# Optimization experiments

Hardware: AMD Instinct MI355X
Metric: run time of the kernel (lower is better)

## Reference

```python
import jax, jax.numpy as jnp
import numpy as np

K = 100  # low-rank dimension


def setup_inputs() -> dict:
    key = jax.random.key(0)
    k1, k2 = jax.random.split(key)
    N, D = 100000, 512
    X = jax.random.normal(k1, (N, D), dtype=jnp.float32)
    # xavier-normal init for Linear(d, 4k): std = sqrt(2/(fan_in+fan_out))
    std = np.sqrt(2.0 / (D + 4 * K)).astype(np.float32)
    W = jax.random.normal(k2, (4 * K, D), dtype=jnp.float32) * std
    b = jnp.zeros((4 * K,), dtype=jnp.float32)
    return {"X": X, "W": W, "b": b}


def reference(X, W, b):
    # tmp = ReLU(X @ W^T + b): [N, 4k]
    tmp = jax.nn.relu(X @ W.T + b)
    U = tmp[:, :K]            # [N, k]
    V = tmp[:, K:2 * K]       # [N, k]
    Z = tmp[:, 2 * K:3 * K]   # [N, k]
    T = tmp[:, 3 * K:]        # [N, k]
    N_rows = X.shape[0]
    # joint_normalize2: sum(U @ (V^T @ ones)) / N + 1e-6 == <colsum(U), colsum(V)> / N + 1e-6
    norm_factor = jnp.dot(jnp.sum(U, axis=0), jnp.sum(V, axis=0)) / N_rows + 1e-6
    Dscale = 1.0 / norm_factor
    # low-rank attention: U @ (V^T @ Z) via small [k, k] intermediate
    VtZ = jnp.einsum('nk,nj->kj', V, Z)   # [k, k]
    res = (U @ VtZ) * Dscale              # [N, k]
    out = jnp.concatenate([res, T], axis=1)  # [N, 2k]
    # dropout p=0.0 (eval-equivalent): identity
    return out
```

## Files before the change

### kernel.cpp

```cpp
#include <hip/hip_runtime.h>
#include <cstdint>

typedef __bf16 bf16;
typedef __attribute__((ext_vector_type(8))) __bf16 bf16x8;
typedef __attribute__((ext_vector_type(4))) __bf16 bf16x4;
typedef __attribute__((ext_vector_type(4))) float f32x4;

#define NROWS 100000
#define DIM   512
#define NC    400
#define NBLK2 521

#define WS_WP    0u
#define WS_SUMU  458752u
#define WS_SUMV  459152u
#define WS_DSC   459552u
#define WS_VTZT  459776u
#define WS_U     524288u
#define WS_PART  66124288u
#define WS_SUMP  71041536u
#define WS_NEED  72291936u

__device__ __forceinline__ void gload_lds16(const void* g, void* l) {
  __builtin_amdgcn_global_load_lds(
      (const __attribute__((address_space(1))) uint32_t*)g,
      (__attribute__((address_space(3))) uint32_t*)l,
      16, 0, 0);
}

__global__ void k1_prep(const float* __restrict__ W, bf16* __restrict__ wp,
                        float* __restrict__ sums) {
  const int idx = blockIdx.x * 256 + threadIdx.x;
  if (idx < 200) sums[idx] = 0.f;
  if (idx >= 16 * 4 * 448 * 8) return;
  const int e = idx & 7;
  int r = idx >> 3;
  const int col = r % 448; r /= 448;
  const int g = r & 3;
  const int t = r >> 2;
  const int k = t * 32 + 4 * g + ((e < 4) ? e : (12 + e));
  wp[idx] = (bf16)((col < NC) ? W[col * DIM + k] : 0.f);
}

__global__ __launch_bounds__(1024) void k2_main(
    const float* __restrict__ X, const bf16* __restrict__ Wp,
    const float* __restrict__ bias, float* __restrict__ out,
    bf16* __restrict__ U, float* __restrict__ part, float* __restrict__ sumP) {
  __shared__ __align__(16) char pool[131072];
  char* Abase0 = pool;
  char* Bbase0 = pool + 73728;

  const int tid  = threadIdx.x;
  const int lane = tid & 63;
  const int wave = tid >> 6;
  const int wm = wave >> 2;
  const int wn = wave & 3;
  const int m  = lane & 15;
  const int g  = lane >> 4;
  const int rb = blockIdx.x * 192;

  f32x4 acc[3][7];
#pragma unroll
  for (int i = 0; i < 3; ++i)
#pragma unroll
    for (int j = 0; j < 7; ++j) acc[i][j] = (f32x4){0.f, 0.f, 0.f, 0.f};

  const int nba = (wave < 8) ? 2 : 1;
  const int ca0 = (wave < 8) ? wave * 2 : 16 + (wave - 8);
  const size_t swb = (size_t)(((lane & 7) ^ (lane >> 3)) * 16);
  int gr0 = rb + ca0 * 8 + (lane >> 3);       if (gr0 > NROWS - 1) gr0 = NROWS - 1;
  int gr1 = rb + (ca0 + 1) * 8 + (lane >> 3); if (gr1 > NROWS - 1) gr1 = NROWS - 1;
  const char* asrc0 = (const char*)X + (size_t)gr0 * 2048 + swb;
  const char* asrc1 = (const char*)X + (size_t)gr1 * 2048 + swb;
  const int nbc = (wave < 12) ? 2 : 1;
  const int bc0 = (wave < 12) ? wave * 2 : 24 + (wave - 12);
  const char* wpc = (const char*)Wp;

#define STAGE_A(T, BUF)                                                        \
  do {                                                                         \
    char* ad = Abase0 + (BUF) * 24576 + ca0 * 1024 + lane * 16;                \
    gload_lds16(asrc0 + (size_t)(T) * 128, ad);                                \
    if (nba == 2) gload_lds16(asrc1 + (size_t)(T) * 128, ad + 1024);           \
  } while (0)
#define STAGE_B(T, BUF)                                                        \
  do {                                                                         \
    const char* bsrc = wpc + (size_t)(T) * 28672;                              \
    for (int q = 0; q < nbc; ++q)                                              \
      gload_lds16(bsrc + (bc0 + q) * 1024 + lane * 16,                         \
                  Bbase0 + (BUF) * 28672 + (bc0 + q) * 1024);                  \
  } while (0)

  STAGE_A(0, 0);
  STAGE_B(0, 0);
  STAGE_A(1, 1);

#pragma unroll
  for (int t = 0; t < 16; ++t) {
    const int ab  = t % 3;
    const int bb_ = t & 1;
    if (t < 15) STAGE_B(t + 1, bb_ ^ 1);
    if (t < 14) STAGE_A(t + 2, (t + 2) % 3);
    if (t < 14) {
      if (wave < 8)       asm volatile("s_waitcnt vmcnt(6)\n\ts_barrier" ::: "memory");
      else if (wave < 12) asm volatile("s_waitcnt vmcnt(4)\n\ts_barrier" ::: "memory");
      else                asm volatile("s_waitcnt vmcnt(3)\n\ts_barrier" ::: "memory");
    } else if (t == 14) {
      if (wave < 8)       asm volatile("s_waitcnt vmcnt(4)\n\ts_barrier" ::: "memory");
      else if (wave < 12) asm volatile("s_waitcnt vmcnt(3)\n\ts_barrier" ::: "memory");
      else                asm volatile("s_waitcnt vmcnt(2)\n\ts_barrier" ::: "memory");
    } else {
      asm volatile("s_waitcnt vmcnt(0)\n\ts_barrier" ::: "memory");
    }

    const int sw = (m & 7) * 16;
    const char* abuf = Abase0 + ab * 24576;
    bf16x8 af[3];
#pragma unroll
    for (int mf = 0; mf < 3; ++mf) {
      const char* rowp = abuf + (wm * 48 + mf * 16 + m) * 128;
      f32x4 alo = *(const f32x4*)(rowp + ((16 * g) ^ sw));
      f32x4 ahi = *(const f32x4*)(rowp + ((64 + 16 * g) ^ sw));
      af[mf] = (bf16x8){(bf16)alo.x, (bf16)alo.y, (bf16)alo.z, (bf16)alo.w,
                        (bf16)ahi.x, (bf16)ahi.y, (bf16)ahi.z, (bf16)ahi.w};
    }

    const bf16* Bc = (const bf16*)(Bbase0 + bb_ * 28672);
#pragma unroll
    for (int nf = 0; nf < 7; ++nf) {
      const int n = wn * 112 + nf * 16 + m;
      bf16x8 bfr = *(const bf16x8*)(Bc + (g * 448 + n) * 8);
#pragma unroll
      for (int mf = 0; mf < 3; ++mf)
        acc[mf][nf] = __builtin_amdgcn_mfma_f32_16x16x32_bf16(af[mf], bfr, acc[mf][nf], 0, 0, 0);
    }
    asm volatile("s_barrier" ::: "memory");
  }
#undef STAGE_A
#undef STAGE_B

  bf16* ldsVZ = (bf16*)pool;
  float* sp   = (float*)(pool + 89600);
  float csum[7];
#pragma unroll
  for (int nf = 0; nf < 7; ++nf) csum[nf] = 0.f;

#pragma unroll
  for (int mf = 0; mf < 3; ++mf) {
#pragma unroll
    for (int nf = 0; nf < 7; ++nf) {
      const int c = wn * 112 + nf * 16 + m;
      const float bv = (c < NC) ? bias[c] : 0.f;
      const int rl0 = wm * 48 + mf * 16 + 4 * g;
      bf16 vz[4];
#pragma unroll
      for (int r = 0; r < 4; ++r) {
        const int row = rb + rl0 + r;
        float v = fmaxf(acc[mf][nf][r] + bv, 0.f);
        const float v2 = (row < NROWS) ? v : 0.f;
        if (row < NROWS) {
          if (c < 100) U[(size_t)row * 128 + c] = (bf16)v;
          if (c >= 300 && c < NC) out[(size_t)row * 200 + 100 + (c - 300)] = v;
        }
        vz[r] = (bf16)v2;
        if (c < 200) csum[nf] += v2;
      }
      if (c >= 100 && c < 300) {
        const int vr = (c < 200) ? (c - 100) : (112 + (c - 200));
        *(bf16x4*)&ldsVZ[(size_t)vr * 200 + rl0] = (bf16x4){vz[0], vz[1], vz[2], vz[3]};
      }
    }
  }
  for (int i = tid; i < 4800; i += 1024) {
    const int rr = (i < 2400) ? (100 + i / 200) : (212 + (i - 2400) / 200);
    ldsVZ[(size_t)rr * 200 + (i % 200)] = (bf16)0.f;
  }
#pragma unroll
  for (int nf = 0; nf < 7; ++nf) {
    float s = csum[nf];
    s += __shfl_xor(s, 16, 64);
    s += __shfl_xor(s, 32, 64);
    if (lane < 16) sp[wave * 112 + nf * 16 + lane] = s;
  }
  __syncthreads();

  if (wave < 7) {
    f32x4 acc2[7];
#pragma unroll
    for (int j = 0; j < 7; ++j) acc2[j] = (f32x4){0.f, 0.f, 0.f, 0.f};
    const bf16* vA = ldsVZ + (size_t)(wave * 16 + m) * 200;
#pragma unroll
    for (int kc = 0; kc < 6; ++kc) {
      bf16x4 a0 = *(const bf16x4*)(vA + kc * 32 + 4 * g);
      bf16x4 a1 = *(const bf16x4*)(vA + kc * 32 + 16 + 4 * g);
      bf16x8 af_ = {a0[0], a0[1], a0[2], a0[3], a1[0], a1[1], a1[2], a1[3]};
#pragma unroll
      for (int fj = 0; fj < 7; ++fj) {
        const bf16* vB = ldsVZ + (size_t)(112 + fj * 16 + m) * 200 + kc * 32;
        bf16x4 b0 = *(const bf16x4*)(vB + 4 * g);
        bf16x4 b1 = *(const bf16x4*)(vB + 16 + 4 * g);
        bf16x8 bf_ = {b0[0], b0[1], b0[2], b0[3], b1[0], b1[1], b1[2], b1[3]};
        acc2[fj] = __builtin_amdgcn_mfma_f32_16x16x32_bf16(af_, bf_, acc2[fj], 0, 0, 0);
      }
    }
    float* pb = part + (size_t)(blockIdx.x % 98) * 12544;
#pragma unroll
    for (int fj = 0; fj < 7; ++fj)
#pragma unroll
      for (int r = 0; r < 4; ++r)
        atomicAdd(&pb[(wave * 16 + 4 * g + r) * 112 + fj * 16 + m], acc2[fj][r]);
  }
  if (tid < 200) {
    const int wq = tid / 112, cc = tid % 112;
    sumP[(size_t)blockIdx.x * 200 + tid] =
        sp[(0 * 4 + wq) * 112 + cc] + sp[(1 * 4 + wq) * 112 + cc] +
        sp[(2 * 4 + wq) * 112 + cc] + sp[(3 * 4 + wq) * 112 + cc];
  }
}

__global__ void k4a0_redsum(const float* __restrict__ sumP,
                            float* __restrict__ sumU, float* __restrict__ sumV) {
  __shared__ float red[4];
  const int c = blockIdx.x;
  const int tid = threadIdx.x;
  float s = 0.f;
  for (int b = tid; b < NBLK2; b += 256) s += sumP[(size_t)b * 200 + c];
#pragma unroll
  for (int off = 1; off < 64; off <<= 1) s += __shfl_xor(s, off, 64);
  if ((tid & 63) == 0) red[tid >> 6] = s;
  __syncthreads();
  if (tid == 0) {
    float t = red[0] + red[1] + red[2] + red[3];
    if (c < 100) sumU[c] = t; else sumV[c - 100] = t;
  }
}

__global__ void k4a_norm(const float* __restrict__ sumU, const float* __restrict__ sumV,
                         float* __restrict__ dsc) {
  const int l = threadIdx.x;
  float v = 0.f;
  if (l < 50) v = sumU[l] * sumV[l] + sumU[l + 50] * sumV[l + 50];
#pragma unroll
  for (int off = 32; off > 0; off >>= 1) v += __shfl_down(v, off, 64);
  if (l == 0) dsc[0] = 1.f / (v * (1.f / (float)NROWS) + 1e-6f);
}

__global__ void k4b_final(const float* __restrict__ part, const float* __restrict__ dsc,
                          bf16* __restrict__ vtzt) {
  const int idx = blockIdx.x * 256 + threadIdx.x;
  if (idx < 1792) vtzt[(idx >> 4) * 128 + 112 + (idx & 15)] = (bf16)0.f;
  if (idx >= 12544) return;
  const int i = idx / 112;
  const int j = idx % 112;
  float s = 0.f;
#pragma unroll 7
  for (int bb = 0; bb < 98; ++bb) s += part[(size_t)bb * 12544 + idx];
  vtzt[j * 128 + i] = (bf16)(s * dsc[0]);
}

__global__ __launch_bounds__(256) void k5_res(
    const bf16* __restrict__ U, const bf16* __restrict__ vtzt,
    float* __restrict__ out) {
  const int tid = threadIdx.x;
  const int lane = tid & 63;
  const int wave = tid >> 6;
  const int m = lane & 15, g = lane >> 4;
  const int rb = blockIdx.x * 128 + wave * 32;

  f32x4 acc[2][7];
#pragma unroll
  for (int i = 0; i < 2; ++i)
#pragma unroll
    for (int j = 0; j < 7; ++j) acc[i][j] = (f32x4){0.f, 0.f, 0.f, 0.f};

  int r0 = rb + m;      if (r0 > NROWS - 1) r0 = NROWS - 1;
  int r1 = rb + 16 + m; if (r1 > NROWS - 1) r1 = NROWS - 1;
  const bf16* u0 = U + (size_t)r0 * 128 + 4 * g;
  const bf16* u1 = U + (size_t)r1 * 128 + 4 * g;
  const bf16* vb = vtzt + 4 * g;

#pragma unroll
  for (int ks = 0; ks < 4; ++ks) {
    bf16x4 A00 = *(const bf16x4*)(u0 + ks * 32);
    bf16x4 A01 = *(const bf16x4*)(u0 + ks * 32 + 16);
    bf16x4 A10 = *(const bf16x4*)(u1 + ks * 32);
    bf16x4 A11 = *(const bf16x4*)(u1 + ks * 32 + 16);
    bf16x8 af0 = {A00[0], A00[1], A00[2], A00[3], A01[0], A01[1], A01[2], A01[3]};
    bf16x8 af1 = {A10[0], A10[1], A10[2], A10[3], A11[0], A11[1], A11[2], A11[3]};
#pragma unroll
    for (int nf = 0; nf < 7; ++nf) {
      const int n = nf * 16 + m;
      bf16x4 B0 = *(const bf16x4*)(vb + n * 128 + ks * 32);
      bf16x4 B1 = *(const bf16x4*)(vb + n * 128 + ks * 32 + 16);
      bf16x8 bfr = {B0[0], B0[1], B0[2], B0[3], B1[0], B1[1], B1[2], B1[3]};
      acc[0][nf] = __builtin_amdgcn_mfma_f32_16x16x32_bf16(af0, bfr, acc[0][nf], 0, 0, 0);
      acc[1][nf] = __builtin_amdgcn_mfma_f32_16x16x32_bf16(af1, bfr, acc[1][nf], 0, 0, 0);
    }
  }
#pragma unroll
  for (int mf = 0; mf < 2; ++mf)
#pragma unroll
    for (int nf = 0; nf < 7; ++nf)
#pragma unroll
      for (int r = 0; r < 4; ++r) {
        const int row = rb + mf * 16 + 4 * g + r;
        const int c = nf * 16 + m;
        if (row < NROWS && c < 100)
          out[(size_t)row * 200 + c] = acc[mf][nf][r];
      }
}

extern "C" void kernel_launch(void* const* d_in, const int* in_sizes, int n_in,
                              void* d_out, int out_size, void* d_ws, size_t ws_size,
                              hipStream_t stream) {
  const float* X = (const float*)d_in[0];
  const float* W = (const float*)d_in[1];
  const float* b = (const float*)d_in[2];
  float* out = (float*)d_out;
  char* ws = (char*)d_ws;
  if (ws_size < WS_NEED) return;

  bf16* wp     = (bf16*)(ws + WS_WP);
  float* sumU  = (float*)(ws + WS_SUMU);
  float* sumV  = (float*)(ws + WS_SUMV);
  float* dsc   = (float*)(ws + WS_DSC);
  bf16* vtzt   = (bf16*)(ws + WS_VTZT);
  bf16* U      = (bf16*)(ws + WS_U);
  float* part  = (float*)(ws + WS_PART);
  float* sumP  = (float*)(ws + WS_SUMP);

  k1_prep<<<896, 256, 0, stream>>>(W, wp, sumU);
  hipMemsetAsync(part, 0, 98u * 12544u * 4u, stream);
  k2_main<<<NBLK2, 1024, 0, stream>>>(X, wp, b, out, U, part, sumP);
  k4a0_redsum<<<200, 256, 0, stream>>>(sumP, sumU, sumV);
  k4a_norm<<<1, 64, 0, stream>>>(sumU, sumV, dsc);
  k4b_final<<<49, 256, 0, stream>>>(part, dsc, vtzt);
  k5_res<<<782, 256, 0, stream>>>(U, vtzt, out);
}
```

Baseline: 208.8 us.

## Use persistent tile loop with triple-buffered A/B staging and MFMA priority

```diff
diff --git a/kernel.cpp b/kernel.cpp
--- a/kernel.cpp
+++ b/kernel.cpp
@@ -9,7 +9,8 @@
 #define NROWS 100000
 #define DIM   512
 #define NC    400
-#define NBLK2 521
+#define NTILE 521
+#define NGRID 512
 
 #define WS_WP    0u
 #define WS_SUMU  458752u
@@ -46,7 +47,7 @@
     const float* __restrict__ X, const bf16* __restrict__ Wp,
     const float* __restrict__ bias, float* __restrict__ out,
     bf16* __restrict__ U, float* __restrict__ part, float* __restrict__ sumP) {
-  __shared__ __align__(16) char pool[131072];
+  __shared__ __align__(16) char pool[159744];
   char* Abase0 = pool;
   char* Bbase0 = pool + 73728;
 
@@ -57,163 +58,159 @@
   const int wn = wave & 3;
   const int m  = lane & 15;
   const int g  = lane >> 4;
-  const int rb = blockIdx.x * 192;
-
-  f32x4 acc[3][7];
-#pragma unroll
-  for (int i = 0; i < 3; ++i)
-#pragma unroll
-    for (int j = 0; j < 7; ++j) acc[i][j] = (f32x4){0.f, 0.f, 0.f, 0.f};
 
   const int nba = (wave < 8) ? 2 : 1;
   const int ca0 = (wave < 8) ? wave * 2 : 16 + (wave - 8);
   const size_t swb = (size_t)(((lane & 7) ^ (lane >> 3)) * 16);
-  int gr0 = rb + ca0 * 8 + (lane >> 3);       if (gr0 > NROWS - 1) gr0 = NROWS - 1;
-  int gr1 = rb + (ca0 + 1) * 8 + (lane >> 3); if (gr1 > NROWS - 1) gr1 = NROWS - 1;
-  const char* asrc0 = (const char*)X + (size_t)gr0 * 2048 + swb;
-  const char* asrc1 = (const char*)X + (size_t)gr1 * 2048 + swb;
   const int nbc = (wave < 12) ? 2 : 1;
   const int bc0 = (wave < 12) ? wave * 2 : 24 + (wave - 12);
   const char* wpc = (const char*)Wp;
 
-#define STAGE_A(T, BUF)                                                        \
-  do {                                                                         \
-    char* ad = Abase0 + (BUF) * 24576 + ca0 * 1024 + lane * 16;                \
-    gload_lds16(asrc0 + (size_t)(T) * 128, ad);                                \
-    if (nba == 2) gload_lds16(asrc1 + (size_t)(T) * 128, ad + 1024);           \
-  } while (0)
-#define STAGE_B(T, BUF)                                                        \
-  do {                                                                         \
-    const char* bsrc = wpc + (size_t)(T) * 28672;                              \
-    for (int q = 0; q < nbc; ++q)                                              \
-      gload_lds16(bsrc + (bc0 + q) * 1024 + lane * 16,                         \
-                  Bbase0 + (BUF) * 28672 + (bc0 + q) * 1024);                  \
-  } while (0)
-
-  STAGE_A(0, 0);
-  STAGE_B(0, 0);
-  STAGE_A(1, 1);
-
-#pragma unroll
-  for (int t = 0; t < 16; ++t) {
-    const int ab  = t % 3;
-    const int bb_ = t & 1;
-    if (t < 15) STAGE_B(t + 1, bb_ ^ 1);
-    if (t < 14) STAGE_A(t + 2, (t + 2) % 3);
-    if (t < 14) {
-      if (wave < 8)       asm volatile("s_waitcnt vmcnt(6)\n\ts_barrier" ::: "memory");
-      else if (wave < 12) asm volatile("s_waitcnt vmcnt(4)\n\ts_barrier" ::: "memory");
-      else                asm volatile("s_waitcnt vmcnt(3)\n\ts_barrier" ::: "memory");
-    } else if (t == 14) {
-      if (wave < 8)       asm volatile("s_waitcnt vmcnt(4)\n\ts_barrier" ::: "memory");
-      else if (wave < 12) asm volatile("s_waitcnt vmcnt(3)\n\ts_barrier" ::: "memory");
-      else                asm volatile("s_waitcnt vmcnt(2)\n\ts_barrier" ::: "memory");
-    } else {
-      asm volatile("s_waitcnt vmcnt(0)\n\ts_barrier" ::: "memory");
-    }
-
-    const int sw = (m & 7) * 16;
-    const char* abuf = Abase0 + ab * 24576;
-    bf16x8 af[3];
+  for (int tile = blockIdx.x; tile < NTILE; tile += NGRID) {
+    const int rb = tile * 192;
+
+    f32x4 acc[3][7];
+#pragma unroll
+    for (int i = 0; i < 3; ++i)
+#pragma unroll
+      for (int j = 0; j < 7; ++j) acc[i][j] = (f32x4){0.f, 0.f, 0.f, 0.f};
+
+    int gr0 = rb + ca0 * 8 + (lane >> 3);       if (gr0 > NROWS - 1) gr0 = NROWS - 1;
+    int gr1 = rb + (ca0 + 1) * 8 + (lane >> 3); if (gr1 > NROWS - 1) gr1 = NROWS - 1;
+    const char* asrc0 = (const char*)X + (size_t)gr0 * 2048 + swb;
+    const char* asrc1 = (const char*)X + (size_t)gr1 * 2048 + swb;
+
+#define STAGE(T, BUF)                                                          \
+    do {                                                                       \
+      char* ad = Abase0 + (BUF) * 24576 + ca0 * 1024 + lane * 16;              \
+      gload_lds16(asrc0 + (size_t)(T) * 128, ad);                              \
+      if (nba == 2) gload_lds16(asrc1 + (size_t)(T) * 128, ad + 1024);         \
+      const char* bsrc = wpc + (size_t)(T) * 28672;                            \
+      for (int q = 0; q < nbc; ++q)                                            \
+        gload_lds16(bsrc + (bc0 + q) * 1024 + lane * 16,                       \
+                    Bbase0 + (BUF) * 28672 + (bc0 + q) * 1024);                \
+    } while (0)
+
+    STAGE(0, 0);
+    STAGE(1, 1);
+
+#pragma unroll
+    for (int t = 0; t < 16; ++t) {
+      const int cur = t % 3;
+      if (t < 15) {
+        if (wave < 8)       asm volatile("s_waitcnt vmcnt(4)\n\ts_barrier" ::: "memory");
+        else if (wave < 12) asm volatile("s_waitcnt vmcnt(3)\n\ts_barrier" ::: "memory");
+        else                asm volatile("s_waitcnt vmcnt(2)\n\ts_barrier" ::: "memory");
+      } else {
+        asm volatile("s_waitcnt vmcnt(0)\n\ts_barrier" ::: "memory");
+      }
+      if (t + 2 < 16) STAGE(t + 2, (t + 2) % 3);
+
+      const int sw = (m & 7) * 16;
+      const char* abuf = Abase0 + cur * 24576;
+      bf16x8 af[3];
+#pragma unroll
+      for (int mf = 0; mf < 3; ++mf) {
+        const char* rowp = abuf + (wm * 48 + mf * 16 + m) * 128;
+        f32x4 alo = *(const f32x4*)(rowp + ((16 * g) ^ sw));
+        f32x4 ahi = *(const f32x4*)(rowp + ((64 + 16 * g) ^ sw));
+        af[mf] = (bf16x8){(bf16)alo.x, (bf16)alo.y, (bf16)alo.z, (bf16)alo.w,
+                          (bf16)ahi.x, (bf16)ahi.y, (bf16)ahi.z, (bf16)ahi.w};
+      }
+
+      const bf16* Bc = (const bf16*)(Bbase0 + cur * 28672);
+      __builtin_amdgcn_s_setprio(1);
+#pragma unroll
+      for (int nf = 0; nf < 7; ++nf) {
+        const int n = wn * 112 + nf * 16 + m;
+        bf16x8 bfr = *(const bf16x8*)(Bc + (g * 448 + n) * 8);
+#pragma unroll
+        for (int mf = 0; mf < 3; ++mf)
+          acc[mf][nf] = __builtin_amdgcn_mfma_f32_16x16x32_bf16(af[mf], bfr, acc[mf][nf], 0, 0, 0);
+      }
+      __builtin_amdgcn_s_setprio(0);
+    }
+#undef STAGE
+    __syncthreads();
+
+    bf16* ldsVZ = (bf16*)pool;
+    float* sp   = (float*)(pool + 89600);
+    float csum[7];
+#pragma unroll
+    for (int nf = 0; nf < 7; ++nf) csum[nf] = 0.f;
+
 #pragma unroll
     for (int mf = 0; mf < 3; ++mf) {
-      const char* rowp = abuf + (wm * 48 + mf * 16 + m) * 128;
-      f32x4 alo = *(const f32x4*)(rowp + ((16 * g) ^ sw));
-      f32x4 ahi = *(const f32x4*)(rowp + ((64 + 16 * g) ^ sw));
-      af[mf] = (bf16x8){(bf16)alo.x, (bf16)alo.y, (bf16)alo.z, (bf16)alo.w,
-                        (bf16)ahi.x, (bf16)ahi.y, (bf16)ahi.z, (bf16)ahi.w};
-    }
-
-    const bf16* Bc = (const bf16*)(Bbase0 + bb_ * 28672);
+#pragma unroll
+      for (int nf = 0; nf < 7; ++nf) {
+        const int c = wn * 112 + nf * 16 + m;
+        const float bv = (c < NC) ? bias[c] : 0.f;
+        const int rl0 = wm * 48 + mf * 16 + 4 * g;
+        bf16 vz[4];
+#pragma unroll
+        for (int r = 0; r < 4; ++r) {
+          const int row = rb + rl0 + r;
+          float v = fmaxf(acc[mf][nf][r] + bv, 0.f);
+          const float v2 = (row < NROWS) ? v : 0.f;
+          if (row < NROWS) {
+            if (c < 100) U[(size_t)row * 128 + c] = (bf16)v;
+            if (c >= 300 && c < NC) out[(size_t)row * 200 + 100 + (c - 300)] = v;
+          }
+          vz[r] = (bf16)v2;
+          if (c < 200) csum[nf] += v2;
+        }
+        if (c >= 100 && c < 300) {
+          const int vr = (c < 200) ? (c - 100) : (112 + (c - 200));
+          *(bf16x4*)&ldsVZ[(size_t)vr * 200 + rl0] = (bf16x4){vz[0], vz[1], vz[2], vz[3]};
+        }
+      }
+    }
+    for (int i = tid; i < 4800; i += 1024) {
+      const int rr = (i < 2400) ? (100 + i / 200) : (212 + (i - 2400) / 200);
+      ldsVZ[(size_t)rr * 200 + (i % 200)] = (bf16)0.f;
+    }
 #pragma unroll
     for (int nf = 0; nf < 7; ++nf) {
-      const int n = wn * 112 + nf * 16 + m;
-      bf16x8 bfr = *(const bf16x8*)(Bc + (g * 448 + n) * 8);
-#pragma unroll
-      for (int mf = 0; mf < 3; ++mf)
-        acc[mf][nf] = __builtin_amdgcn_mfma_f32_16x16x32_bf16(af[mf], bfr, acc[mf][nf], 0, 0, 0);
-    }
-    asm volatile("s_barrier" ::: "memory");
-  }
-#undef STAGE_A
-#undef STAGE_B
-
-  bf16* ldsVZ = (bf16*)pool;
-  float* sp   = (float*)(pool + 89600);
-  float csum[7];
-#pragma unroll
-  for (int nf = 0; nf < 7; ++nf) csum[nf] = 0.f;
-
-#pragma unroll
-  for (int mf = 0; mf < 3; ++mf) {
-#pragma unroll
-    for (int nf = 0; nf < 7; ++nf) {
-      const int c = wn * 112 + nf * 16 + m;
-      const float bv = (c < NC) ? bias[c] : 0.f;
-      const int rl0 = wm * 48 + mf * 16 + 4 * g;
-      bf16 vz[4];
-#pragma unroll
-      for (int r = 0; r < 4; ++r) {
-        const int row = rb + rl0 + r;
-        float v = fmaxf(acc[mf][nf][r] + bv, 0.f);
-        const float v2 = (row < NROWS) ? v : 0.f;
-        if (row < NROWS) {
-          if (c < 100) U[(size_t)row * 128 + c] = (bf16)v;
-          if (c >= 300 && c < NC) out[(size_t)row * 200 + 100 + (c - 300)] = v;
+      float s = csum[nf];
+      s += __shfl_xor(s, 16, 64);
+      s += __shfl_xor(s, 32, 64);
+      if (lane < 16) sp[wave * 112 + nf * 16 + lane] = s;
+    }
+    __syncthreads();
+
+    if (wave < 7) {
+      f32x4 acc2[7];
+#pragma unroll
+      for (int j = 0; j < 7; ++j) acc2[j] = (f32x4){0.f, 0.f, 0.f, 0.f};
+      const bf16* vA = ldsVZ + (size_t)(wave * 16 + m) * 200;
+#pragma unroll
+      for (int kc = 0; kc < 6; ++kc) {
+        bf16x4 a0 = *(const bf16x4*)(vA + kc * 32 + 4 * g);
+        bf16x4 a1 = *(const bf16x4*)(vA + kc * 32 + 16 + 4 * g);
+        bf16x8 af_ = {a0[0], a0[1], a0[2], a0[3], a1[0], a1[1], a1[2], a1[3]};
+#pragma unroll
+        for (int fj = 0; fj < 7; ++fj) {
+          const bf16* vB = ldsVZ + (size_t)(112 + fj * 16 + m) * 200 + kc * 32;
+          bf16x4 b0 = *(const bf16x4*)(vB + 4 * g);
+          bf16x4 b1 = *(const bf16x4*)(vB + 16 + 4 * g);
+          bf16x8 bf_ = {b0[0], b0[1], b0[2], b0[3], b1[0], b1[1], b1[2], b1[3]};
+          acc2[fj] = __builtin_amdgcn_mfma_f32_16x16x32_bf16(af_, bf_, acc2[fj], 0, 0, 0);
         }
-        vz[r] = (bf16)v2;
-        if (c < 200) csum[nf] += v2;
-      }
-      if (c >= 100 && c < 300) {
-        const int vr = (c < 200) ? (c - 100) : (112 + (c - 200));
-        *(bf16x4*)&ldsVZ[(size_t)vr * 200 + rl0] = (bf16x4){vz[0], vz[1], vz[2], vz[3]};
-      }
-    }
-  }
-  for (int i = tid; i < 4800; i += 1024) {
-    const int rr = (i < 2400) ? (100 + i / 200) : (212 + (i - 2400) / 200);
-    ldsVZ[(size_t)rr * 200 + (i % 200)] = (bf16)0.f;
-  }
-#pragma unroll
-  for (int nf = 0; nf < 7; ++nf) {
-    float s = csum[nf];
-    s += __shfl_xor(s, 16, 64);
-    s += __shfl_xor(s, 32, 64);
-    if (lane < 16) sp[wave * 112 + nf * 16 + lane] = s;
-  }
-  __syncthreads();
-
-  if (wave < 7) {
-    f32x4 acc2[7];
-#pragma unroll
-    for (int j = 0; j < 7; ++j) acc2[j] = (f32x4){0.f, 0.f, 0.f, 0.f};
-    const bf16* vA = ldsVZ + (size_t)(wave * 16 + m) * 200;
-#pragma unroll
-    for (int kc = 0; kc < 6; ++kc) {
-      bf16x4 a0 = *(const bf16x4*)(vA + kc * 32 + 4 * g);
-      bf16x4 a1 = *(const bf16x4*)(vA + kc * 32 + 16 + 4 * g);
-      bf16x8 af_ = {a0[0], a0[1], a0[2], a0[3], a1[0], a1[1], a1[2], a1[3]};
-#pragma unroll
-      for (int fj = 0; fj < 7; ++fj) {
-        const bf16* vB = ldsVZ + (size_t)(112 + fj * 16 + m) * 200 + kc * 32;
-        bf16x4 b0 = *(const bf16x4*)(vB + 4 * g);
-        bf16x4 b1 = *(const bf16x4*)(vB + 16 + 4 * g);
-        bf16x8 bf_ = {b0[0], b0[1], b0[2], b0[3], b1[0], b1[1], b1[2], b1[3]};
-        acc2[fj] = __builtin_amdgcn_mfma_f32_16x16x32_bf16(af_, bf_, acc2[fj], 0, 0, 0);
-      }
-    }
-    float* pb = part + (size_t)(blockIdx.x % 98) * 12544;
-#pragma unroll
-    for (int fj = 0; fj < 7; ++fj)
-#pragma unroll
-      for (int r = 0; r < 4; ++r)
-        atomicAdd(&pb[(wave * 16 + 4 * g + r) * 112 + fj * 16 + m], acc2[fj][r]);
-  }
-  if (tid < 200) {
-    const int wq = tid / 112, cc = tid % 112;
-    sumP[(size_t)blockIdx.x * 200 + tid] =
-        sp[(0 * 4 + wq) * 112 + cc] + sp[(1 * 4 + wq) * 112 + cc] +
-        sp[(2 * 4 + wq) * 112 + cc] + sp[(3 * 4 + wq) * 112 + cc];
+      }
+      float* pb = part + (size_t)(tile % 98) * 12544;
+#pragma unroll
+      for (int fj = 0; fj < 7; ++fj)
+#pragma unroll
+        for (int r = 0; r < 4; ++r)
+          atomicAdd(&pb[(wave * 16 + 4 * g + r) * 112 + fj * 16 + m], acc2[fj][r]);
+    }
+    if (tid < 200) {
+      const int wq = tid / 112, cc = tid % 112;
+      sumP[(size_t)tile * 200 + tid] =
+          sp[(0 * 4 + wq) * 112 + cc] + sp[(1 * 4 + wq) * 112 + cc] +
+          sp[(2 * 4 + wq) * 112 + cc] + sp[(3 * 4 + wq) * 112 + cc];
+    }
+    __syncthreads();
   }
 }
 
@@ -223,7 +220,7 @@
   const int c = blockIdx.x;
   const int tid = threadIdx.x;
   float s = 0.f;
-  for (int b = tid; b < NBLK2; b += 256) s += sumP[(size_t)b * 200 + c];
+  for (int b = tid; b < NTILE; b += 256) s += sumP[(size_t)b * 200 + c];
 #pragma unroll
   for (int off = 1; off < 64; off <<= 1) s += __shfl_xor(s, off, 64);
   if ((tid & 63) == 0) red[tid >> 6] = s;
@@ -330,7 +327,7 @@
 
   k1_prep<<<896, 256, 0, stream>>>(W, wp, sumU);
   hipMemsetAsync(part, 0, 98u * 12544u * 4u, stream);
-  k2_main<<<NBLK2, 1024, 0, stream>>>(X, wp, b, out, U, part, sumP);
+  k2_main<<<NGRID, 1024, 0, stream>>>(X, wp, b, out, U, part, sumP);
   k4a0_redsum<<<200, 256, 0, stream>>>(sumP, sumU, sumV);
   k4a_norm<<<1, 64, 0, stream>>>(sumU, sumV, dsc);
   k4b_final<<<49, 256, 0, stream>>>(part, dsc, vtzt);
```

Result: slower. 350.0 us (+67.7%).
